# Optimization experiments

Hardware: AMD Instinct MI355X
Metric: run time of the kernel (lower is better)

The kernel has to match this reference:

```python
import jax, jax.numpy as jnp
import numpy as np

N, D, K = 100000, 512, 32
H1, H2 = 512, 256
LN2PI_2 = float(np.log(2.0 * np.pi) / 2.0)


def _glorot(key, shape):
    fan_in, fan_out = shape[0], shape[1]
    limit = np.sqrt(6.0 / (fan_in + fan_out))
    return jax.random.uniform(key, shape, jnp.float32, -limit, limit)


def setup_inputs() -> dict:
    key = jax.random.key(0)
    k0, k1, k2, k3 = jax.random.split(key, 4)
    return {
        "x": jax.random.normal(k0, (N, D), jnp.float32),
        "W1": _glorot(k1, (D, H1)),
        "b1": jnp.zeros((H1,), jnp.float32),
        "W2": _glorot(k2, (H1, H2)),
        "b2": jnp.zeros((H2,), jnp.float32),
        "W3": _glorot(k3, (H2, K)),
        "b3": jnp.zeros((K,), jnp.float32),
    }


def reference(x, W1, b1, W2, b2, W3, b3):
    # instance attention MLP: softplus hiddens, softmax output -> [N, K]
    h = jax.nn.softplus(x @ W1 + b1)
    h = jax.nn.softplus(h @ W2 + b2)
    att = jax.nn.softmax(h @ W3 + b3, axis=-1)

    att_sum = jnp.sum(att, axis=0)  # [K]
    # weighted mean: sum_n x[n,d] * att[n,k] / sum_n att[n,k]  -> [K, D]
    means = (att.T @ x) / att_sum[:, None]
    # weighted variance: E_w[x^2] - mean^2 (algebraic expansion of
    # sum_n (x - mean)^2 * att / sum att, avoids [N,K,D] intermediate)
    ex2 = (att.T @ (x * x)) / att_sum[:, None]  # [K, D]
    vars_ = ex2 - means * means

    # GMM diagonal log-likelihood, expanded to GEMM form:
    inv_v = 1.0 / vars_  # [K, D]
    maha = (x * x) @ inv_v.T - 2.0 * (x @ (means * inv_v).T) \
           + jnp.sum(means * means * inv_v, axis=-1)[None, :]  # [N, K]
    gmm_log = -0.5 * maha - 0.5 * jnp.sum(jnp.log(vars_), axis=-1)[None, :] - D * LN2PI_2
    return gmm_log, vars_
```

## Files before the change

### kernel.cpp

```cpp
#include <hip/hip_runtime.h>
#include <hip/hip_bf16.h>
#include <math.h>

#define NROWS 100000
#define DDIM  512
#define KCL   32
#define H1DIM 512
#define H2DIM 256
#define LN2PI_2 0.9189385332046727f
#define NCHUNK 196
#define NPAD  100352
#define NBLK2 1568

typedef __attribute__((ext_vector_type(8))) short short8;
typedef __attribute__((ext_vector_type(4))) short shortx4;
typedef __attribute__((ext_vector_type(4))) float floatx4;

__device__ __forceinline__ float softplus_f(float v) {
    return fmaxf(v, 0.f) + __logf(1.f + __expf(-fabsf(v)));
}

__device__ __forceinline__ unsigned short f2bf_rne(float f) {
    unsigned int u = __float_as_uint(f);
    return (unsigned short)((u + 0x7fffu + ((u >> 16) & 1u)) >> 16);
}

__device__ __forceinline__ float bf2f(short v) {
    return __uint_as_float(((unsigned int)(unsigned short)v) << 16);
}

__global__ __launch_bounds__(256) void cvt_x_bf16(
    const float* __restrict__ x, short* __restrict__ xb)
{
    size_t i = ((size_t)blockIdx.x * 256 + threadIdx.x) * 8;
    float4 f0 = *(const float4*)&x[i];
    float4 f1 = *(const float4*)&x[i + 4];
    short8 o;
    o[0] = (short)f2bf_rne(f0.x); o[1] = (short)f2bf_rne(f0.y);
    o[2] = (short)f2bf_rne(f0.z); o[3] = (short)f2bf_rne(f0.w);
    o[4] = (short)f2bf_rne(f1.x); o[5] = (short)f2bf_rne(f1.y);
    o[6] = (short)f2bf_rne(f1.z); o[7] = (short)f2bf_rne(f1.w);
    *(short8*)&xb[i] = o;
}

__global__ __launch_bounds__(256) void cvt_weights(
    const float* __restrict__ W1, const float* __restrict__ W2,
    const float* __restrict__ W3, short* __restrict__ W1T,
    short* __restrict__ W2T, short* __restrict__ W3T)
{
    int idx = blockIdx.x * 256 + threadIdx.x;
    const int n1 = DDIM * H1DIM;
    const int n2 = H1DIM * H2DIM;
    const int n3 = H2DIM * KCL;
    if (idx < n1) {
        int n = idx % H1DIM, k = idx / H1DIM;
        W1T[(size_t)n * DDIM + k] = (short)f2bf_rne(W1[idx]);
    } else if (idx < n1 + n2) {
        int rel = idx - n1;
        int n = rel % H2DIM, k = rel / H2DIM;
        W2T[(size_t)n * H1DIM + k] = (short)f2bf_rne(W2[rel]);
    } else if (idx < n1 + n2 + n3) {
        int rel = idx - n1 - n2;
        int n = rel % KCL, k = rel / KCL;
        W3T[(size_t)n * H2DIM + k] = (short)f2bf_rne(W3[rel]);
    }
}

#define LDP 40
__global__ __launch_bounds__(256) void gemm_sp(
    const short* __restrict__ A, const short* __restrict__ BT,
    const float* __restrict__ bias, short* __restrict__ Cptr,
    int M, int Nc, int Kd)
{
    __shared__ short As[2][128 * LDP];
    __shared__ short Bs[2][128 * LDP];

    const int tid = threadIdx.x;
    const int lid = tid & 63;
    const int w = tid >> 6;
    const int lm = lid & 15;
    const int lq = lid >> 4;
    const int wrow = (w & 1) * 64;
    const int wcol = (w >> 1) * 64;

    const int row0 = blockIdx.y * 128;
    const int col0 = blockIdx.x * 128;

    const int sr = tid >> 2;
    const int sc = (tid & 3) << 3;

    int gr0 = row0 + sr;       if (gr0 >= M) gr0 = M - 1;
    int gr1 = row0 + 64 + sr;  if (gr1 >= M) gr1 = M - 1;
    const short* Ar0 = A + (size_t)gr0 * Kd + sc;
    const short* Ar1 = A + (size_t)gr1 * Kd + sc;
    const short* Br0 = BT + (size_t)(col0 + sr) * Kd + sc;
    const short* Br1 = BT + (size_t)(col0 + 64 + sr) * Kd + sc;

    floatx4 acc[4][4];
    #pragma unroll
    for (int i = 0; i < 4; i++)
        #pragma unroll
        for (int j = 0; j < 4; j++)
            acc[i][j] = (floatx4){0.f, 0.f, 0.f, 0.f};

    short8 pa0, pa1, pb0, pb1;
    pa0 = *(const short8*)Ar0;
    pa1 = *(const short8*)Ar1;
    pb0 = *(const short8*)Br0;
    pb1 = *(const short8*)Br1;

    const int nk = Kd >> 5;
    for (int kt = 0; kt < nk; kt++) {
        const int buf = kt & 1;
        *(short8*)&As[buf][sr * LDP + sc]        = pa0;
        *(short8*)&As[buf][(64 + sr) * LDP + sc] = pa1;
        *(short8*)&Bs[buf][sr * LDP + sc]        = pb0;
        *(short8*)&Bs[buf][(64 + sr) * LDP + sc] = pb1;
        if (kt + 1 < nk) {
            int ko = (kt + 1) << 5;
            pa0 = *(const short8*)(Ar0 + ko);
            pa1 = *(const short8*)(Ar1 + ko);
            pb0 = *(const short8*)(Br0 + ko);
            pb1 = *(const short8*)(Br1 + ko);
        }
        __syncthreads();

        short8 a[4], b[4];
        #pragma unroll
        for (int i = 0; i < 4; i++)
            a[i] = *(const short8*)&As[buf][(wrow + i * 16 + lm) * LDP + lq * 8];
        #pragma unroll
        for (int j = 0; j < 4; j++)
            b[j] = *(const short8*)&Bs[buf][(wcol + j * 16 + lm) * LDP + lq * 8];
        #pragma unroll
        for (int i = 0; i < 4; i++)
            #pragma unroll
            for (int j = 0; j < 4; j++)
                acc[i][j] = __builtin_amdgcn_mfma_f32_16x16x32_bf16(
                    a[i], b[j], acc[i][j], 0, 0, 0);
    }

    float bb[4];
    #pragma unroll
    for (int j = 0; j < 4; j++)
        bb[j] = bias[col0 + wcol + j * 16 + lm];

    #pragma unroll
    for (int i = 0; i < 4; i++) {
        #pragma unroll
        for (int reg = 0; reg < 4; reg++) {
            int rr = row0 + wrow + i * 16 + lq * 4 + reg;
            if (rr < M) {
                #pragma unroll
                for (int j = 0; j < 4; j++) {
                    int c = col0 + wcol + j * 16 + lm;
                    float v = softplus_f(acc[i][j][reg] + bb[j]);
                    Cptr[(size_t)rr * Nc + c] = (short)f2bf_rne(v);
                }
            }
        }
    }
}

__global__ __launch_bounds__(256) void gemm2_logits(
    const short* __restrict__ h1, const short* __restrict__ W2T,
    const float* __restrict__ b2, const short* __restrict__ W3T,
    const float* __restrict__ b3, short* __restrict__ attT,
    float* __restrict__ Patt)
{
    __shared__ __align__(16) short lds[25600];
    __shared__ float red[4][32];

    short* AsB = lds;
    short* BsB = lds + 2 * 64 * LDP;

    const int tid = threadIdx.x;
    const int lid = tid & 63;
    const int w = tid >> 6;
    const int lm = lid & 15;
    const int lq = lid >> 4;
    const int wcol = w * 64;

    const int row0 = blockIdx.x * 64;

    const int sr = tid >> 2;
    const int sc = (tid & 3) << 3;

    int gr = row0 + sr; if (gr >= NROWS) gr = NROWS - 1;
    const short* Ar  = h1  + (size_t)gr * H1DIM + sc;
    const short* Br0 = W2T + (size_t)sr * H1DIM + sc;
    const short* Br1 = W2T + (size_t)(64 + sr) * H1DIM + sc;
    const short* Br2 = W2T + (size_t)(128 + sr) * H1DIM + sc;
    const short* Br3 = W2T + (size_t)(192 + sr) * H1DIM + sc;

    floatx4 acc[4][4];
    #pragma unroll
    for (int i = 0; i < 4; i++)
        #pragma unroll
        for (int j = 0; j < 4; j++)
            acc[i][j] = (floatx4){0.f, 0.f, 0.f, 0.f};

    short8 pa, pb0, pb1, pb2, pb3;
    pa  = *(const short8*)Ar;
    pb0 = *(const short8*)Br0;
    pb1 = *(const short8*)Br1;
    pb2 = *(const short8*)Br2;
    pb3 = *(const short8*)Br3;

    const int nk = H1DIM >> 5;
    for (int kt = 0; kt < nk; kt++) {
        const int buf = kt & 1;
        *(short8*)&AsB[buf * (64 * LDP) + sr * LDP + sc]          = pa;
        *(short8*)&BsB[buf * (256 * LDP) + sr * LDP + sc]         = pb0;
        *(short8*)&BsB[buf * (256 * LDP) + (64 + sr) * LDP + sc]  = pb1;
        *(short8*)&BsB[buf * (256 * LDP) + (128 + sr) * LDP + sc] = pb2;
        *(short8*)&BsB[buf * (256 * LDP) + (192 + sr) * LDP + sc] = pb3;
        if (kt + 1 < nk) {
            int ko = (kt + 1) << 5;
            pa  = *(const short8*)(Ar + ko);
            pb0 = *(const short8*)(Br0 + ko);
            pb1 = *(const short8*)(Br1 + ko);
            pb2 = *(const short8*)(Br2 + ko);
            pb3 = *(const short8*)(Br3 + ko);
        }
        __syncthreads();

        short8 a[4], b[4];
        #pragma unroll
        for (int i = 0; i < 4; i++)
            a[i] = *(const short8*)&AsB[buf * (64 * LDP) + (i * 16 + lm) * LDP + lq * 8];
        #pragma unroll
        for (int j = 0; j < 4; j++)
            b[j] = *(const short8*)&BsB[buf * (256 * LDP) + (wcol + j * 16 + lm) * LDP + lq * 8];
        #pragma unroll
        for (int i = 0; i < 4; i++)
            #pragma unroll
            for (int j = 0; j < 4; j++)
                acc[i][j] = __builtin_amdgcn_mfma_f32_16x16x32_bf16(
                    a[i], b[j], acc[i][j], 0, 0, 0);
    }

    __syncthreads();

    float bb2[4];
    #pragma unroll
    for (int j = 0; j < 4; j++)
        bb2[j] = b2[wcol + j * 16 + lm];
    #pragma unroll
    for (int i = 0; i < 4; i++) {
        #pragma unroll
        for (int reg = 0; reg < 4; reg++) {
            const int r = i * 16 + lq * 4 + reg;
            const int rx = (r & 7) << 4;
            #pragma unroll
            for (int j = 0; j < 4; j++) {
                const int c = wcol + j * 16 + lm;
                float v = softplus_f(acc[i][j][reg] + bb2[j]);
                *(short*)((char*)lds + ((r * 512 + c * 2) ^ rx)) =
                    (short)f2bf_rne(v);
            }
        }
    }
    __syncthreads();

    short8 bf3[2][8];
    #pragma unroll
    for (int j = 0; j < 2; j++)
        #pragma unroll
        for (int s = 0; s < 8; s++)
            bf3[j][s] = *(const short8*)&W3T[(j * 16 + lm) * H2DIM + s * 32 + lq * 8];

    floatx4 lacc[2];
    lacc[0] = (floatx4){0.f, 0.f, 0.f, 0.f};
    lacc[1] = (floatx4){0.f, 0.f, 0.f, 0.f};
    const int lr = w * 16 + lm;
    const int lrx = (lr & 7) << 4;
    #pragma unroll
    for (int s = 0; s < 8; s++) {
        short8 a0 = *(const short8*)((const char*)lds +
                        ((lr * 512 + s * 64 + lq * 16) ^ lrx));
        lacc[0] = __builtin_amdgcn_mfma_f32_16x16x32_bf16(a0, bf3[0][s], lacc[0], 0, 0, 0);
        lacc[1] = __builtin_amdgcn_mfma_f32_16x16x32_bf16(a0, bf3[1][s], lacc[1], 0, 0, 0);
    }

    const float b3v0 = b3[lm];
    const float b3v1 = b3[16 + lm];
    float p0 = 0.f, p1 = 0.f;
    float e0s[4], e1s[4];
    #pragma unroll
    for (int reg = 0; reg < 4; reg++) {
        const int rg = row0 + w * 16 + lq * 4 + reg;
        float v0 = lacc[0][reg] + b3v0;
        float v1 = lacc[1][reg] + b3v1;
        float m = fmaxf(v0, v1);
        m = fmaxf(m, __shfl_xor(m, 1));
        m = fmaxf(m, __shfl_xor(m, 2));
        m = fmaxf(m, __shfl_xor(m, 4));
        m = fmaxf(m, __shfl_xor(m, 8));
        float e0 = __expf(v0 - m);
        float e1 = __expf(v1 - m);
        float sm = e0 + e1;
        sm += __shfl_xor(sm, 1);
        sm += __shfl_xor(sm, 2);
        sm += __shfl_xor(sm, 4);
        sm += __shfl_xor(sm, 8);
        float inv = 1.f / sm;
        e0 *= inv; e1 *= inv;
        if (rg >= NROWS) { e0 = 0.f; e1 = 0.f; }
        p0 += e0; p1 += e1;
        e0s[reg] = e0; e1s[reg] = e1;
    }
    p0 += __shfl_xor(p0, 16); p0 += __shfl_xor(p0, 32);
    p1 += __shfl_xor(p1, 16); p1 += __shfl_xor(p1, 32);
    if (lq == 0) { red[w][lm] = p0; red[w][16 + lm] = p1; }

    __syncthreads();

    short (*Ts)[72] = (short(*)[72])lds;
    #pragma unroll
    for (int reg = 0; reg < 4; reg++) {
        const int rloc = w * 16 + lq * 4 + reg;
        Ts[lm][rloc]      = (short)f2bf_rne(e0s[reg]);
        Ts[16 + lm][rloc] = (short)f2bf_rne(e1s[reg]);
    }
    __syncthreads();

    if (tid < KCL)
        Patt[blockIdx.x * KCL + tid] =
            red[0][tid] + red[1][tid] + red[2][tid] + red[3][tid];

    {
        int rr = tid >> 3;
        int cs = (tid & 7) << 3;
        *(short8*)&attT[(size_t)rr * NPAD + row0 + cs] =
            *(const short8*)&Ts[rr][cs];
    }
}

__global__ __launch_bounds__(256, 4) void stats_mfma(
    const short* __restrict__ xb, const short* __restrict__ attT,
    float* __restrict__ P)
{
    __shared__ short xT[32 * 512];

    const int tid = threadIdx.x;
    const int lane = tid & 63;
    const int lm = lane & 15;
    const int lq = lane >> 4;
    const int w = tid >> 6;
    const int kh = w >> 1;
    const int dh = w & 1;

    const int cblk = blockIdx.x;
    const int dgrp = blockIdx.y;
    const int n0 = cblk * 512;

    short8 afrag[16];
    const short* arow = attT + (size_t)(kh * 16 + lm) * NPAD + n0 + lq * 8;
    #pragma unroll
    for (int s = 0; s < 16; s++)
        afrag[s] = *(const short8*)(arow + s * 32);

    const int c = tid & 31;
    const int rq = tid >> 5;
    const bool full = (n0 + 512 <= NROWS);

    for (int dt = 0; dt < 4; dt++) {
        const int colf = dgrp * 128 + dt * 32 + c;
        __syncthreads();
        if (full) {
            const short* xp = xb + (size_t)n0 * DDIM + colf;
            #pragma unroll 4
            for (int p = 0; p < 16; p++) {
                int rr = p * 32 + rq * 4;
                unsigned int h0 = (unsigned short)xp[(size_t)(rr + 0) * DDIM];
                unsigned int h1 = (unsigned short)xp[(size_t)(rr + 1) * DDIM];
                unsigned int h2 = (unsigned short)xp[(size_t)(rr + 2) * DDIM];
                unsigned int h3 = (unsigned short)xp[(size_t)(rr + 3) * DDIM];
                int boff = (c << 10) + ((rr * 2) ^ ((c & 15) << 4));
                *(uint2*)((char*)xT + boff) =
                    make_uint2(h0 | (h1 << 16), h2 | (h3 << 16));
            }
        } else {
            #pragma unroll 4
            for (int p = 0; p < 16; p++) {
                int rr = p * 32 + rq * 4;
                int g0 = min(n0 + rr + 0, NROWS - 1);
                int g1 = min(n0 + rr + 1, NROWS - 1);
                int g2 = min(n0 + rr + 2, NROWS - 1);
                int g3 = min(n0 + rr + 3, NROWS - 1);
                unsigned int h0 = (unsigned short)xb[(size_t)g0 * DDIM + colf];
                unsigned int h1 = (unsigned short)xb[(size_t)g1 * DDIM + colf];
                unsigned int h2 = (unsigned short)xb[(size_t)g2 * DDIM + colf];
                unsigned int h3 = (unsigned short)xb[(size_t)g3 * DDIM + colf];
                int boff = (c << 10) + ((rr * 2) ^ ((c & 15) << 4));
                *(uint2*)((char*)xT + boff) =
                    make_uint2(h0 | (h1 << 16), h2 | (h3 << 16));
            }
        }
        __syncthreads();

        floatx4 acc1 = (floatx4){0.f, 0.f, 0.f, 0.f};
        floatx4 acc2 = (floatx4){0.f, 0.f, 0.f, 0.f};
        const int rowb = (dh * 16 + lm) << 10;
        #pragma unroll
        for (int s = 0; s < 16; s++) {
            int boff = rowb + ((s * 64 + lq * 16) ^ (lm << 4));
            short8 bx = *(const short8*)((const char*)xT + boff);
            union { short8 s8; unsigned int u[4]; } bq;
            #pragma unroll
            for (int e = 0; e < 4; e++) {
                float f0 = bf2f(bx[2 * e]);
                float f1 = bf2f(bx[2 * e + 1]);
                f0 *= f0; f1 *= f1;
                bq.u[e] = (unsigned int)f2bf_rne(f0) |
                          ((unsigned int)f2bf_rne(f1) << 16);
            }
            acc1 = __builtin_amdgcn_mfma_f32_16x16x32_bf16(
                afrag[s], bx, acc1, 0, 0, 0);
            acc2 = __builtin_amdgcn_mfma_f32_16x16x32_bf16(
                afrag[s], bq.s8, acc2, 0, 0, 0);
        }

        const size_t pbase = (size_t)cblk * 32768 +
                             (size_t)(kh * 16 + lq * 4) * 512 +
                             (size_t)(dgrp * 128 + dt * 32 + dh * 16 + lm);
        #pragma unroll
        for (int reg = 0; reg < 4; reg++) {
            P[pbase + (size_t)reg * 512]         = acc1[reg];
            P[pbase + 16384 + (size_t)reg * 512] = acc2[reg];
        }
    }
}

__global__ __launch_bounds__(256) void stats_reduce(
    const float* __restrict__ P, const float* __restrict__ Patt,
    float* __restrict__ S12, float* __restrict__ att_sum)
{
    int e = blockIdx.x * 256 + threadIdx.x;
    float sum = 0.f;
    for (int cc = 0; cc < NCHUNK; cc++)
        sum += P[(size_t)cc * 32768 + e];
    S12[e] = sum;

    if (blockIdx.x == 0 && threadIdx.x < KCL) {
        float as = 0.f;
        for (int cc = 0; cc < NBLK2; cc++) as += Patt[cc * KCL + threadIdx.x];
        att_sum[threadIdx.x] = as;
    }
}

__global__ __launch_bounds__(256) void finalize_stats(
    const float* __restrict__ S12, const float* __restrict__ att_sum,
    short* __restrict__ Bp, float* __restrict__ konst,
    float* __restrict__ vars_out)
{
    int k = blockIdx.x;
    int tid = threadIdx.x;
    __shared__ float red[256];

    float inv_as = 1.f / att_sum[k];
    float csum = 0.f, lsum = 0.f;
    for (int d = tid; d < DDIM; d += 256) {
        float mean = S12[k * DDIM + d] * inv_as;
        float ex2  = S12[KCL * DDIM + k * DDIM + d] * inv_as;
        float var  = ex2 - mean * mean;
        vars_out[k * DDIM + d] = var;
        float iv = 1.f / var;
        Bp[(size_t)k * 1024 + d]       = (short)f2bf_rne(-0.5f * iv);
        Bp[(size_t)k * 1024 + 512 + d] = (short)f2bf_rne(mean * iv);
        csum += mean * mean * iv;
        lsum += logf(var);
    }
    red[tid] = csum;
    __syncthreads();
    for (int s = 128; s > 0; s >>= 1) {
        if (tid < s) red[tid] += red[tid + s];
        __syncthreads();
    }
    float ctot = red[0];
    __syncthreads();
    red[tid] = lsum;
    __syncthreads();
    for (int s = 128; s > 0; s >>= 1) {
        if (tid < s) red[tid] += red[tid + s];
        __syncthreads();
    }
    if (tid == 0)
        konst[k] = -0.5f * ctot - 0.5f * red[0] - DDIM * LN2PI_2;
}

#define LDG 40
__global__ __launch_bounds__(256) void gmm_out_mfma(
    const short* __restrict__ xb, const short* __restrict__ Bp,
    const float* __restrict__ konst, float* __restrict__ out)
{
    __shared__ short As_sq[256 * LDG];
    __shared__ short As_x[256 * LDG];

    const int tid = threadIdx.x;
    const int lane = tid & 63;
    const int lm = lane & 15;
    const int lq = lane >> 4;
    const int wid = tid >> 6;
    const int row0 = blockIdx.x * 256;

    floatx4 acc[4][2];
    #pragma unroll
    for (int i = 0; i < 4; i++)
        #pragma unroll
        for (int j = 0; j < 2; j++)
            acc[i][j] = (floatx4){0.f, 0.f, 0.f, 0.f};

    int rrh[8], segh[8], grh[8];
    bool okh[8];
    #pragma unroll
    for (int h = 0; h < 8; h++) {
        int u = tid + h * 256;
        rrh[h] = u >> 3;
        segh[h] = (u & 7) << 2;
        int gr = row0 + rrh[h];
        okh[h] = (gr < NROWS);
        grh[h] = okh[h] ? gr : 0;
    }

    shortx4 pf[8];
    #pragma unroll
    for (int h = 0; h < 8; h++) {
        shortx4 v = (shortx4){0, 0, 0, 0};
        if (okh[h]) v = *(const shortx4*)&xb[(size_t)grh[h] * DDIM + segh[h]];
        pf[h] = v;
    }

    for (int dt = 0; dt < 16; dt++) {
        __syncthreads();
        #pragma unroll
        for (int h = 0; h < 8; h++) {
            shortx4 sx = pf[h];
            shortx4 sq;
            #pragma unroll
            for (int e = 0; e < 4; e++) {
                float f = bf2f(sx[e]);
                sq[e] = (short)f2bf_rne(f * f);
            }
            *(shortx4*)&As_x[rrh[h] * LDG + segh[h]]  = sx;
            *(shortx4*)&As_sq[rrh[h] * LDG + segh[h]] = sq;
        }
        if (dt + 1 < 16) {
            #pragma unroll
            for (int h = 0; h < 8; h++) {
                shortx4 v = (shortx4){0, 0, 0, 0};
                if (okh[h])
                    v = *(const shortx4*)&xb[(size_t)grh[h] * DDIM +
                                             (dt + 1) * 32 + segh[h]];
                pf[h] = v;
            }
        }
        __syncthreads();

        short8 a_sq[4], a_x[4], b_sq[2], b_x[2];
        #pragma unroll
        for (int i = 0; i < 4; i++) {
            int off = (wid * 64 + i * 16 + lm) * LDG + lq * 8;
            a_sq[i] = *(const short8*)&As_sq[off];
            a_x[i]  = *(const short8*)&As_x[off];
        }
        #pragma unroll
        for (int j = 0; j < 2; j++) {
            const size_t bo = (size_t)(j * 16 + lm) * 1024 + dt * 32 + lq * 8;
            b_sq[j] = *(const short8*)&Bp[bo];
            b_x[j]  = *(const short8*)&Bp[bo + 512];
        }
        #pragma unroll
        for (int i = 0; i < 4; i++)
            #pragma unroll
            for (int j = 0; j < 2; j++) {
                acc[i][j] = __builtin_amdgcn_mfma_f32_16x16x32_bf16(
                    a_sq[i], b_sq[j], acc[i][j], 0, 0, 0);
                acc[i][j] = __builtin_amdgcn_mfma_f32_16x16x32_bf16(
                    a_x[i], b_x[j], acc[i][j], 0, 0, 0);
            }
    }

    float kst[2];
    kst[0] = konst[lm];
    kst[1] = konst[16 + lm];

    #pragma unroll
    for (int i = 0; i < 4; i++) {
        #pragma unroll
        for (int reg = 0; reg < 4; reg++) {
            int rr = row0 + wid * 64 + i * 16 + lq * 4 + reg;
            if (rr < NROWS) {
                out[(size_t)rr * KCL + lm]      = acc[i][0][reg] + kst[0];
                out[(size_t)rr * KCL + 16 + lm] = acc[i][1][reg] + kst[1];
            }
        }
    }
}

extern "C" void kernel_launch(void* const* d_in, const int* in_sizes, int n_in,
                              void* d_out, int out_size, void* d_ws, size_t ws_size,
                              hipStream_t stream)
{
    const float* x  = (const float*)d_in[0];
    const float* W1 = (const float*)d_in[1];
    const float* b1 = (const float*)d_in[2];
    const float* W2 = (const float*)d_in[3];
    const float* b2 = (const float*)d_in[4];
    const float* W3 = (const float*)d_in[5];
    const float* b3 = (const float*)d_in[6];
    float* out = (float*)d_out;

    short* h1b     = (short*)d_ws;
    float* h2      = (float*)(h1b + (size_t)NROWS * H1DIM);
    float* att     = h2 + (size_t)NROWS * H2DIM;
    float* P       = att + (size_t)NROWS * KCL;
    float* PattOld = P + (size_t)NCHUNK * 32768;
    float* S12     = PattOld + NCHUNK * KCL;
    float* att_sum = S12 + 2 * KCL * DDIM;
    short* Bp      = (short*)(att_sum + KCL);
    float* konst   = (float*)(Bp + KCL * 1024);
    (void)ws_size; (void)in_sizes; (void)n_in; (void)out_size; (void)PattOld;

    short* xb = (short*)h2;
    short* attT  = (short*)att;
    float* PattN = (float*)(attT + (size_t)KCL * NPAD);
    short* W1T = (short*)P;
    short* W2T = W1T + H1DIM * DDIM;
    short* W3T = W2T + H2DIM * H1DIM;

    cvt_x_bf16<<<dim3(NROWS * DDIM / 2048), 256, 0, stream>>>(x, xb);
    cvt_weights<<<dim3(1568), 256, 0, stream>>>(W1, W2, W3, W1T, W2T, W3T);

    int mblocks = (NROWS + 127) / 128;

    gemm_sp<<<dim3(H1DIM / 128, mblocks), 256, 0, stream>>>(
        xb, W1T, b1, h1b, NROWS, H1DIM, DDIM);
    gemm2_logits<<<dim3(NBLK2), 256, 0, stream>>>(
        h1b, W2T, b2, W3T, b3, attT, PattN);
    stats_mfma<<<dim3(NCHUNK, 4), 256, 0, stream>>>(xb, attT, P);
    stats_reduce<<<dim3(128), 256, 0, stream>>>(P, PattN, S12, att_sum);
    finalize_stats<<<dim3(KCL), 256, 0, stream>>>(
        S12, att_sum, Bp, konst, out + (size_t)NROWS * KCL);
    gmm_out_mfma<<<dim3((NROWS + 255) / 256), 256, 0, stream>>>(
        xb, Bp, konst, out);
}
```

Measured before the change: 611.0 us.

## Enlarge GEMM tiles to 512-thread blocks in first and second MLP layers

Both MLP GEMM kernels now run with 512-thread blocks (8 waves). The layer-1 GEMM computes 128x256 output tiles instead of 128x128, and the layer-2/logits kernel processes 128 rows per block instead of 64. Waves are rearranged into a 2x4 grid, and the epilogue transposes, reductions and block counts are adjusted to match. The goal is to reload the activation and weight tiles less often from global memory, at the cost of more LDS per block and possibly lower occupancy.

Result: faster. 590.4 us (-3.4%).

```diff
diff --git a/kernel.cpp b/kernel.cpp
--- a/kernel.cpp
+++ b/kernel.cpp
@@ -10,7 +10,7 @@
 #define LN2PI_2 0.9189385332046727f
 #define NCHUNK 196
 #define NPAD  100352
-#define NBLK2 1568
+#define NBLKL 784
 
 typedef __attribute__((ext_vector_type(8))) short short8;
 typedef __attribute__((ext_vector_type(4))) short shortx4;
@@ -67,13 +67,13 @@
 }
 
 #define LDP 40
-__global__ __launch_bounds__(256) void gemm_sp(
+__global__ __launch_bounds__(512) void gemm_sp(
     const short* __restrict__ A, const short* __restrict__ BT,
     const float* __restrict__ bias, short* __restrict__ Cptr,
     int M, int Nc, int Kd)
 {
     __shared__ short As[2][128 * LDP];
-    __shared__ short Bs[2][128 * LDP];
+    __shared__ short Bs[2][256 * LDP];
 
     const int tid = threadIdx.x;
     const int lid = tid & 63;
@@ -84,17 +84,15 @@
     const int wcol = (w >> 1) * 64;
 
     const int row0 = blockIdx.y * 128;
-    const int col0 = blockIdx.x * 128;
+    const int col0 = blockIdx.x * 256;
 
     const int sr = tid >> 2;
     const int sc = (tid & 3) << 3;
 
-    int gr0 = row0 + sr;       if (gr0 >= M) gr0 = M - 1;
-    int gr1 = row0 + 64 + sr;  if (gr1 >= M) gr1 = M - 1;
-    const short* Ar0 = A + (size_t)gr0 * Kd + sc;
-    const short* Ar1 = A + (size_t)gr1 * Kd + sc;
+    int gr = row0 + sr; if (gr >= M) gr = M - 1;
+    const short* Ar  = A + (size_t)gr * Kd + sc;
     const short* Br0 = BT + (size_t)(col0 + sr) * Kd + sc;
-    const short* Br1 = BT + (size_t)(col0 + 64 + sr) * Kd + sc;
+    const short* Br1 = BT + (size_t)(col0 + 128 + sr) * Kd + sc;
 
     floatx4 acc[4][4];
     #pragma unroll
@@ -103,23 +101,20 @@
         for (int j = 0; j < 4; j++)
             acc[i][j] = (floatx4){0.f, 0.f, 0.f, 0.f};
 
-    short8 pa0, pa1, pb0, pb1;
-    pa0 = *(const short8*)Ar0;
-    pa1 = *(const short8*)Ar1;
+    short8 pa, pb0, pb1;
+    pa  = *(const short8*)Ar;
     pb0 = *(const short8*)Br0;
     pb1 = *(const short8*)Br1;
 
     const int nk = Kd >> 5;
     for (int kt = 0; kt < nk; kt++) {
         const int buf = kt & 1;
-        *(short8*)&As[buf][sr * LDP + sc]        = pa0;
-        *(short8*)&As[buf][(64 + sr) * LDP + sc] = pa1;
-        *(short8*)&Bs[buf][sr * LDP + sc]        = pb0;
-        *(short8*)&Bs[buf][(64 + sr) * LDP + sc] = pb1;
+        *(short8*)&As[buf][sr * LDP + sc]         = pa;
+        *(short8*)&Bs[buf][sr * LDP + sc]         = pb0;
+        *(short8*)&Bs[buf][(128 + sr) * LDP + sc] = pb1;
         if (kt + 1 < nk) {
             int ko = (kt + 1) << 5;
-            pa0 = *(const short8*)(Ar0 + ko);
-            pa1 = *(const short8*)(Ar1 + ko);
+            pa  = *(const short8*)(Ar + ko);
             pb0 = *(const short8*)(Br0 + ko);
             pb1 = *(const short8*)(Br1 + ko);
         }
@@ -162,26 +157,27 @@
     }
 }
 
-__global__ __launch_bounds__(256) void gemm2_logits(
+__global__ __launch_bounds__(512) void gemm2_logits(
     const short* __restrict__ h1, const short* __restrict__ W2T,
     const float* __restrict__ b2, const short* __restrict__ W3T,
     const float* __restrict__ b3, short* __restrict__ attT,
     float* __restrict__ Patt)
 {
-    __shared__ __align__(16) short lds[25600];
-    __shared__ float red[4][32];
+    __shared__ __align__(16) short lds[32768];
+    __shared__ float red[8][32];
 
     short* AsB = lds;
-    short* BsB = lds + 2 * 64 * LDP;
+    short* BsB = lds + 2 * 128 * LDP;
 
     const int tid = threadIdx.x;
     const int lid = tid & 63;
     const int w = tid >> 6;
     const int lm = lid & 15;
     const int lq = lid >> 4;
-    const int wcol = w * 64;
-
-    const int row0 = blockIdx.x * 64;
+    const int wrow = (w & 1) * 64;
+    const int wcol = (w >> 1) * 64;
+
+    const int row0 = blockIdx.x * 128;
 
     const int sr = tid >> 2;
     const int sc = (tid & 3) << 3;
@@ -189,9 +185,7 @@
     int gr = row0 + sr; if (gr >= NROWS) gr = NROWS - 1;
     const short* Ar  = h1  + (size_t)gr * H1DIM + sc;
     const short* Br0 = W2T + (size_t)sr * H1DIM + sc;
-    const short* Br1 = W2T + (size_t)(64 + sr) * H1DIM + sc;
-    const short* Br2 = W2T + (size_t)(128 + sr) * H1DIM + sc;
-    const short* Br3 = W2T + (size_t)(192 + sr) * H1DIM + sc;
+    const short* Br1 = W2T + (size_t)(128 + sr) * H1DIM + sc;
 
     floatx4 acc[4][4];
     #pragma unroll
@@ -200,35 +194,29 @@
         for (int j = 0; j < 4; j++)
             acc[i][j] = (floatx4){0.f, 0.f, 0.f, 0.f};
 
-    short8 pa, pb0, pb1, pb2, pb3;
+    short8 pa, pb0, pb1;
     pa  = *(const short8*)Ar;
     pb0 = *(const short8*)Br0;
     pb1 = *(const short8*)Br1;
-    pb2 = *(const short8*)Br2;
-    pb3 = *(const short8*)Br3;
 
     const int nk = H1DIM >> 5;
     for (int kt = 0; kt < nk; kt++) {
         const int buf = kt & 1;
-        *(short8*)&AsB[buf * (64 * LDP) + sr * LDP + sc]          = pa;
+        *(short8*)&AsB[buf * (128 * LDP) + sr * LDP + sc]         = pa;
         *(short8*)&BsB[buf * (256 * LDP) + sr * LDP + sc]         = pb0;
-        *(short8*)&BsB[buf * (256 * LDP) + (64 + sr) * LDP + sc]  = pb1;
-        *(short8*)&BsB[buf * (256 * LDP) + (128 + sr) * LDP + sc] = pb2;
-        *(short8*)&BsB[buf * (256 * LDP) + (192 + sr) * LDP + sc] = pb3;
+        *(short8*)&BsB[buf * (256 * LDP) + (128 + sr) * LDP + sc] = pb1;
         if (kt + 1 < nk) {
             int ko = (kt + 1) << 5;
             pa  = *(const short8*)(Ar + ko);
             pb0 = *(const short8*)(Br0 + ko);
             pb1 = *(const short8*)(Br1 + ko);
-            pb2 = *(const short8*)(Br2 + ko);
-            pb3 = *(const short8*)(Br3 + ko);
         }
         __syncthreads();
 
         short8 a[4], b[4];
         #pragma unroll
         for (int i = 0; i < 4; i++)
-            a[i] = *(const short8*)&AsB[buf * (64 * LDP) + (i * 16 + lm) * LDP + lq * 8];
+            a[i] = *(const short8*)&AsB[buf * (128 * LDP) + (wrow + i * 16 + lm) * LDP + lq * 8];
         #pragma unroll
         for (int j = 0; j < 4; j++)
             b[j] = *(const short8*)&BsB[buf * (256 * LDP) + (wcol + j * 16 + lm) * LDP + lq * 8];
@@ -250,7 +238,7 @@
     for (int i = 0; i < 4; i++) {
         #pragma unroll
         for (int reg = 0; reg < 4; reg++) {
-            const int r = i * 16 + lq * 4 + reg;
+            const int r = wrow + i * 16 + lq * 4 + reg;
             const int rx = (r & 7) << 4;
             #pragma unroll
             for (int j = 0; j < 4; j++) {
@@ -316,7 +304,7 @@
 
     __syncthreads();
 
-    short (*Ts)[72] = (short(*)[72])lds;
+    short (*Ts)[136] = (short(*)[136])lds;
     #pragma unroll
     for (int reg = 0; reg < 4; reg++) {
         const int rloc = w * 16 + lq * 4 + reg;
@@ -325,13 +313,16 @@
     }
     __syncthreads();
 
-    if (tid < KCL)
-        Patt[blockIdx.x * KCL + tid] =
-            red[0][tid] + red[1][tid] + red[2][tid] + red[3][tid];
+    if (tid < KCL) {
+        float ps = 0.f;
+        #pragma unroll
+        for (int ww = 0; ww < 8; ww++) ps += red[ww][tid];
+        Patt[blockIdx.x * KCL + tid] = ps;
+    }
 
     {
-        int rr = tid >> 3;
-        int cs = (tid & 7) << 3;
+        int rr = tid >> 4;
+        int cs = (tid & 15) << 3;
         *(short8*)&attT[(size_t)rr * NPAD + row0 + cs] =
             *(const short8*)&Ts[rr][cs];
     }
@@ -445,7 +436,7 @@
 
     if (blockIdx.x == 0 && threadIdx.x < KCL) {
         float as = 0.f;
-        for (int cc = 0; cc < NBLK2; cc++) as += Patt[cc * KCL + threadIdx.x];
+        for (int cc = 0; cc < NBLKL; cc++) as += Patt[cc * KCL + threadIdx.x];
         att_sum[threadIdx.x] = as;
     }
 }
@@ -635,9 +626,9 @@
 
     int mblocks = (NROWS + 127) / 128;
 
-    gemm_sp<<<dim3(H1DIM / 128, mblocks), 256, 0, stream>>>(
+    gemm_sp<<<dim3(H1DIM / 256, mblocks), 512, 0, stream>>>(
         xb, W1T, b1, h1b, NROWS, H1DIM, DDIM);
-    gemm2_logits<<<dim3(NBLK2), 256, 0, stream>>>(
+    gemm2_logits<<<dim3(NBLKL), 512, 0, stream>>>(
         h1b, W2T, b2, W3T, b3, attT, PattN);
     stats_mfma<<<dim3(NCHUNK, 4), 256, 0, stream>>>(xb, attT, P);
     stats_reduce<<<dim3(128), 256, 0, stream>>>(P, PattN, S12, att_sum);
```
